# Performance work log

Measured on AMD Instinct MI355X. Metric: run time of the kernel, lower is better.

## Reference

```python
import jax, jax.numpy as jnp
import numpy as np

N_NODES = 100000
N_EDGES = 1600000
IN_CH, HID_CH, OUT_CH = 128, 64, 40


def setup_inputs() -> dict:
    key = jax.random.key(0)
    k_x, k_e, k_w1, k_w2 = jax.random.split(key, 4)
    x = jax.random.normal(k_x, (N_NODES, IN_CH), dtype=jnp.float32)
    edge_index = jax.random.randint(k_e, (2, N_EDGES), 0, N_NODES, dtype=jnp.int64)
    # Glorot-ish scaled weights, zero bias (matches GCNConv init convention)
    W1 = jax.random.normal(k_w1, (IN_CH, HID_CH), dtype=jnp.float32) / np.sqrt(IN_CH)
    b1 = jnp.zeros((HID_CH,), dtype=jnp.float32)
    W2 = jax.random.normal(k_w2, (HID_CH, OUT_CH), dtype=jnp.float32) / np.sqrt(HID_CH)
    b2 = jnp.zeros((OUT_CH,), dtype=jnp.float32)
    return {"x": x, "edge_index": edge_index, "W1": W1, "b1": b1, "W2": W2, "b2": b2}


def _gcn_conv(x, edge_index, W, b, n):
    """GCNConv with normalize=True: linear transform, add self-loops,
    symmetric D^-1/2 A D^-1/2 aggregation (source_to_target flow), bias."""
    h = x @ W  # [n, out]
    loops = jnp.arange(n, dtype=edge_index.dtype)
    row = jnp.concatenate([edge_index[0], loops])  # sources
    col = jnp.concatenate([edge_index[1], loops])  # targets
    deg = jax.ops.segment_sum(jnp.ones_like(col, dtype=h.dtype), col, num_segments=n)
    dinv = jnp.where(deg > 0, jax.lax.rsqrt(deg), jnp.zeros_like(deg))
    w = dinv[row] * dinv[col]  # [E+n] per-edge norm
    out = jax.ops.segment_sum(h[row] * w[:, None], col, num_segments=n)  # scatter-add to targets
    return out + b


def reference(x, edge_index, W1, b1, W2, b2):
    # eval mode: F.dropout(p=0.8, training=False) is identity
    n = x.shape[0]
    h = jax.nn.relu(_gcn_conv(x, edge_index, W1, b1, n))
    return _gcn_conv(h, edge_index, W2, b2, n)  # [N, OUT_CH] logits
```

## Files before the change

kernel.cpp:

```cpp
#include <hip/hip_runtime.h>

#define N_NODES 100000
#define N_EDGES 1600000
#define IN_CH   128
#define HID_CH  64
#define OUT_CH  40
#define NBKT    391
#define EPB     4096
#define CAP     6144

using bf16x8 = __attribute__((ext_vector_type(8))) short;
using f32x4  = __attribute__((ext_vector_type(4))) float;

__device__ __forceinline__ float bf2f(unsigned short u) {
    union { unsigned int i; float f; } c; c.i = ((unsigned int)u) << 16; return c.f;
}
__device__ __forceinline__ unsigned short f2bf(float f) {
    union { float f; unsigned int i; } c; c.f = f;
    unsigned int r = c.i + 0x7FFFu + ((c.i >> 16) & 1u);
    return (unsigned short)(r >> 16);
}
__device__ __forceinline__ float4 bf2f4(ushort4 u) {
    return make_float4(bf2f(u.x), bf2f(u.y), bf2f(u.z), bf2f(u.w));
}

__global__ void k_setup(const float* __restrict__ W1, const float* __restrict__ W2,
                        unsigned short* __restrict__ W1t, unsigned short* __restrict__ W2t,
                        int* __restrict__ gcur) {
    int stride = gridDim.x * blockDim.x;
    int t0 = blockIdx.x * blockDim.x + threadIdx.x;
    if (t0 < NBKT) gcur[t0] = t0 * CAP;
    for (int i = t0; i < 64 * 128; i += stride) {
        int n = i >> 7, k = i & 127;
        W1t[i] = f2bf(W1[k * 64 + n]);
    }
    for (int i = t0; i < 48 * 64; i += stride) {
        int n = i >> 6, k = i & 63;
        W2t[i] = f2bf(n < 40 ? W2[k * 40 + n] : 0.0f);
    }
}

__global__ void k_bin(const int* __restrict__ ei, int* __restrict__ gcur,
                      int* __restrict__ ebuf) {
    __shared__ int hist[NBKT];
    __shared__ int lcur[NBKT];
    int tid = threadIdx.x;
    int base = blockIdx.x * EPB;
    int nloc = N_EDGES - base;
    if (nloc > EPB) nloc = EPB;
    int n4 = nloc >> 2;
    const int4* S4 = (const int4*)(ei + base);
    const int4* D4 = (const int4*)(ei + N_EDGES + base);

    for (int i = tid; i < NBKT; i += 256) hist[i] = 0;
    __syncthreads();
    for (int i = tid; i < n4; i += 256) {
        int4 d = D4[i];
        atomicAdd(&hist[d.x >> 8], 1);
        atomicAdd(&hist[d.y >> 8], 1);
        atomicAdd(&hist[d.z >> 8], 1);
        atomicAdd(&hist[d.w >> 8], 1);
    }
    __syncthreads();
    for (int i = tid; i < NBKT; i += 256) {
        int h = hist[i];
        lcur[i] = h ? atomicAdd(&gcur[i], h) : 0;
    }
    __syncthreads();
    for (int i = tid; i < n4; i += 256) {
        int4 s = S4[i];
        int4 d = D4[i];
        int p;
        p = atomicAdd(&lcur[d.x >> 8], 1); ebuf[p] = s.x | ((d.x & 255) << 20);
        p = atomicAdd(&lcur[d.y >> 8], 1); ebuf[p] = s.y | ((d.y & 255) << 20);
        p = atomicAdd(&lcur[d.z >> 8], 1); ebuf[p] = s.z | ((d.z & 255) << 20);
        p = atomicAdd(&lcur[d.w >> 8], 1); ebuf[p] = s.w | ((d.w & 255) << 20);
    }
}

__global__ void k_node(const int* __restrict__ gcur, const int* __restrict__ ebuf,
                       int* __restrict__ row_start, int* __restrict__ row_end,
                       int* __restrict__ csr_src, float* __restrict__ dinv) {
    __shared__ int cnt[256];
    __shared__ int s[256];
    int tid = threadIdx.x;
    int b = blockIdx.x;
    int node0 = b << 8;
    int lo = b * CAP, hi = gcur[b];
    int n = hi - lo, n4 = n >> 2;
    const int4* E4 = (const int4*)(ebuf + lo);

    cnt[tid] = 0;
    __syncthreads();
    for (int i = tid; i < n4; i += 256) {
        int4 w = E4[i];
        atomicAdd(&cnt[(unsigned)w.x >> 20], 1);
        atomicAdd(&cnt[(unsigned)w.y >> 20], 1);
        atomicAdd(&cnt[(unsigned)w.z >> 20], 1);
        atomicAdd(&cnt[(unsigned)w.w >> 20], 1);
    }
    for (int e = lo + (n4 << 2) + tid; e < hi; e += 256)
        atomicAdd(&cnt[(unsigned)ebuf[e] >> 20], 1);
    __syncthreads();
    int c = cnt[tid];
    s[tid] = c;
    __syncthreads();
#pragma unroll
    for (int off = 1; off < 256; off <<= 1) {
        int tv = (tid >= off) ? s[tid - off] : 0;
        __syncthreads();
        s[tid] += tv;
        __syncthreads();
    }
    int node = node0 + tid;
    if (node < N_NODES) {
        row_start[node] = lo + s[tid] - c;
        row_end[node]   = lo + s[tid];
        dinv[node] = rsqrtf(1.0f + (float)c);
    }
    __syncthreads();
    cnt[tid] = lo + s[tid] - c;
    __syncthreads();
    for (int i = tid; i < n4; i += 256) {
        int4 w = E4[i];
        int p;
        p = atomicAdd(&cnt[(unsigned)w.x >> 20], 1); csr_src[p] = w.x & 0xFFFFF;
        p = atomicAdd(&cnt[(unsigned)w.y >> 20], 1); csr_src[p] = w.y & 0xFFFFF;
        p = atomicAdd(&cnt[(unsigned)w.z >> 20], 1); csr_src[p] = w.z & 0xFFFFF;
        p = atomicAdd(&cnt[(unsigned)w.w >> 20], 1); csr_src[p] = w.w & 0xFFFFF;
    }
    for (int e = lo + (n4 << 2) + tid; e < hi; e += 256) {
        int w = ebuf[e];
        int p = atomicAdd(&cnt[(unsigned)w >> 20], 1);
        csr_src[p] = w & 0xFFFFF;
    }
}

__global__ __launch_bounds__(256, 4)
void k_gemm1(const float* __restrict__ x, const unsigned short* __restrict__ W1t,
             const float* __restrict__ dinv, unsigned short* __restrict__ h1s) {
    __shared__ unsigned short Al[64 * 136];
    __shared__ unsigned short Bl[64 * 136];
    __shared__ float dl[64];
    int tid = threadIdx.x;
    long long node0 = (long long)blockIdx.x * 64;

    const float4* X = (const float4*)x;
    for (int i = tid; i < 64 * 32; i += 256) {
        int r = i >> 5, c4 = i & 31;
        long long gr = node0 + r;
        if (gr >= N_NODES) gr = N_NODES - 1;
        float4 v = X[gr * 32 + c4];
        *(ushort4*)&Al[r * 136 + c4 * 4] =
            make_ushort4(f2bf(v.x), f2bf(v.y), f2bf(v.z), f2bf(v.w));
    }
    for (int i = tid; i < 64 * 16; i += 256) {
        int nn = i >> 4, c8 = i & 15;
        *(ulonglong2*)&Bl[nn * 136 + c8 * 8] = *(const ulonglong2*)&W1t[nn * 128 + c8 * 8];
    }
    if (tid < 64) {
        long long gr = node0 + tid;
        dl[tid] = dinv[gr < N_NODES ? gr : N_NODES - 1];
    }
    __syncthreads();

    int lane = tid & 63, wave = tid >> 6;
    int quad = lane >> 4, l16 = lane & 15;
    int arow = wave * 16 + l16;
    f32x4 ac0 = {0,0,0,0}, ac1 = {0,0,0,0}, ac2 = {0,0,0,0}, ac3 = {0,0,0,0};

#pragma unroll
    for (int ks = 0; ks < 4; ++ks) {
        int ko = ks * 32 + quad * 8;
        bf16x8 a  = *(const bf16x8*)&Al[arow * 136 + ko];
        bf16x8 b0 = *(const bf16x8*)&Bl[( 0 + l16) * 136 + ko];
        bf16x8 b1 = *(const bf16x8*)&Bl[(16 + l16) * 136 + ko];
        bf16x8 b2 = *(const bf16x8*)&Bl[(32 + l16) * 136 + ko];
        bf16x8 b3 = *(const bf16x8*)&Bl[(48 + l16) * 136 + ko];
        ac0 = __builtin_amdgcn_mfma_f32_16x16x32_bf16(a, b0, ac0, 0, 0, 0);
        ac1 = __builtin_amdgcn_mfma_f32_16x16x32_bf16(a, b1, ac1, 0, 0, 0);
        ac2 = __builtin_amdgcn_mfma_f32_16x16x32_bf16(a, b2, ac2, 0, 0, 0);
        ac3 = __builtin_amdgcn_mfma_f32_16x16x32_bf16(a, b3, ac3, 0, 0, 0);
    }

#pragma unroll
    for (int r = 0; r < 4; ++r) {
        int rl = wave * 16 + quad * 4 + r;
        long long grow = node0 + rl;
        if (grow < N_NODES) {
            float dd = dl[rl];
            h1s[grow * 64 +  0 + l16] = f2bf(ac0[r] * dd);
            h1s[grow * 64 + 16 + l16] = f2bf(ac1[r] * dd);
            h1s[grow * 64 + 32 + l16] = f2bf(ac2[r] * dd);
            h1s[grow * 64 + 48 + l16] = f2bf(ac3[r] * dd);
        }
    }
}

__global__ void k_agg1(const int* __restrict__ row_start, const int* __restrict__ row_end,
                       const int* __restrict__ csr_src,
                       const unsigned short* __restrict__ h1s, const float* __restrict__ dinv,
                       const float* __restrict__ b1, unsigned short* __restrict__ a1b) {
    int idx = blockIdx.x * blockDim.x + threadIdx.x;
    int node = idx >> 4;
    int cg = idx & 15;
    if (node >= N_NODES) return;
    int e = row_start[node];
    int f = row_end[node];
    const ushort4* H = (const ushort4*)h1s;
    float4 acc = bf2f4(H[(long long)node * 16 + cg]);
    float4 acc2 = {0.f, 0.f, 0.f, 0.f};
    while (f - e >= 8) {
        int s0 = csr_src[e];
        int s1 = csr_src[e + 1];
        int s2 = csr_src[e + 2];
        int s3 = csr_src[e + 3];
        int t0 = csr_src[f - 4];
        int t1 = csr_src[f - 3];
        int t2 = csr_src[f - 2];
        int t3 = csr_src[f - 1];
        float4 v0 = bf2f4(H[(long long)s0 * 16 + cg]);
        float4 v1 = bf2f4(H[(long long)s1 * 16 + cg]);
        float4 v2 = bf2f4(H[(long long)s2 * 16 + cg]);
        float4 v3 = bf2f4(H[(long long)s3 * 16 + cg]);
        float4 u0 = bf2f4(H[(long long)t0 * 16 + cg]);
        float4 u1 = bf2f4(H[(long long)t1 * 16 + cg]);
        float4 u2 = bf2f4(H[(long long)t2 * 16 + cg]);
        float4 u3 = bf2f4(H[(long long)t3 * 16 + cg]);
        acc.x  += (v0.x + v1.x) + (v2.x + v3.x);
        acc.y  += (v0.y + v1.y) + (v2.y + v3.y);
        acc.z  += (v0.z + v1.z) + (v2.z + v3.z);
        acc.w  += (v0.w + v1.w) + (v2.w + v3.w);
        acc2.x += (u0.x + u1.x) + (u2.x + u3.x);
        acc2.y += (u0.y + u1.y) + (u2.y + u3.y);
        acc2.z += (u0.z + u1.z) + (u2.z + u3.z);
        acc2.w += (u0.w + u1.w) + (u2.w + u3.w);
        e += 4; f -= 4;
    }
    for (; e < f; ++e) {
        float4 v = bf2f4(H[(long long)csr_src[e] * 16 + cg]);
        acc.x += v.x; acc.y += v.y; acc.z += v.z; acc.w += v.w;
    }
    acc.x += acc2.x; acc.y += acc2.y; acc.z += acc2.z; acc.w += acc2.w;
    float dd = dinv[node];
    float4 bb = ((const float4*)b1)[cg];
    float rx = fmaxf(acc.x * dd + bb.x, 0.f);
    float ry = fmaxf(acc.y * dd + bb.y, 0.f);
    float rz = fmaxf(acc.z * dd + bb.z, 0.f);
    float rw = fmaxf(acc.w * dd + bb.w, 0.f);
    ((ushort4*)a1b)[(long long)node * 16 + cg] =
        make_ushort4(f2bf(rx), f2bf(ry), f2bf(rz), f2bf(rw));
}

__global__ __launch_bounds__(256, 4)
void k_gemm2(const unsigned short* __restrict__ a1b, const unsigned short* __restrict__ W2t,
             const float* __restrict__ dinv, unsigned short* __restrict__ h2s) {
    __shared__ unsigned short Al[64 * 72];
    __shared__ unsigned short Bl[48 * 72];
    __shared__ float dl[64];
    int tid = threadIdx.x;
    long long node0 = (long long)blockIdx.x * 64;

    for (int i = tid; i < 64 * 8; i += 256) {
        int r = i >> 3, c8 = i & 7;
        long long gr = node0 + r;
        if (gr >= N_NODES) gr = N_NODES - 1;
        *(ulonglong2*)&Al[r * 72 + c8 * 8] = *(const ulonglong2*)&a1b[gr * 64 + c8 * 8];
    }
    for (int i = tid; i < 48 * 8; i += 256) {
        int nn = i >> 3, c8 = i & 7;
        *(ulonglong2*)&Bl[nn * 72 + c8 * 8] = *(const ulonglong2*)&W2t[nn * 64 + c8 * 8];
    }
    if (tid < 64) {
        long long gr = node0 + tid;
        dl[tid] = dinv[gr < N_NODES ? gr : N_NODES - 1];
    }
    __syncthreads();

    int lane = tid & 63, wave = tid >> 6;
    int quad = lane >> 4, l16 = lane & 15;
    int arow = wave * 16 + l16;
    f32x4 ac0 = {0,0,0,0}, ac1 = {0,0,0,0}, ac2 = {0,0,0,0};

#pragma unroll
    for (int ks = 0; ks < 2; ++ks) {
        int ko = ks * 32 + quad * 8;
        bf16x8 a  = *(const bf16x8*)&Al[arow * 72 + ko];
        bf16x8 b0 = *(const bf16x8*)&Bl[( 0 + l16) * 72 + ko];
        bf16x8 b1v = *(const bf16x8*)&Bl[(16 + l16) * 72 + ko];
        bf16x8 b2 = *(const bf16x8*)&Bl[(32 + l16) * 72 + ko];
        ac0 = __builtin_amdgcn_mfma_f32_16x16x32_bf16(a, b0, ac0, 0, 0, 0);
        ac1 = __builtin_amdgcn_mfma_f32_16x16x32_bf16(a, b1v, ac1, 0, 0, 0);
        ac2 = __builtin_amdgcn_mfma_f32_16x16x32_bf16(a, b2, ac2, 0, 0, 0);
    }

#pragma unroll
    for (int r = 0; r < 4; ++r) {
        int rl = wave * 16 + quad * 4 + r;
        long long grow = node0 + rl;
        if (grow < N_NODES) {
            float dd = dl[rl];
            h2s[grow * 40 +  0 + l16] = f2bf(ac0[r] * dd);
            h2s[grow * 40 + 16 + l16] = f2bf(ac1[r] * dd);
            if (l16 < 8) h2s[grow * 40 + 32 + l16] = f2bf(ac2[r] * dd);
        }
    }
}

__global__ void k_agg2(const int* __restrict__ row_start, const int* __restrict__ row_end,
                       const int* __restrict__ csr_src,
                       const unsigned short* __restrict__ h2s, const float* __restrict__ dinv,
                       const float* __restrict__ b2, float* __restrict__ out) {
    int idx = blockIdx.x * blockDim.x + threadIdx.x;
    int node = idx >> 4;
    int cg = idx & 15;
    if (node >= N_NODES || cg >= 10) return;
    int e = row_start[node];
    int f = row_end[node];
    const ushort4* H = (const ushort4*)h2s;
    float4 acc = bf2f4(H[(long long)node * 10 + cg]);
    float4 acc2 = {0.f, 0.f, 0.f, 0.f};
    while (f - e >= 8) {
        int s0 = csr_src[e];
        int s1 = csr_src[e + 1];
        int s2 = csr_src[e + 2];
        int s3 = csr_src[e + 3];
        int t0 = csr_src[f - 4];
        int t1 = csr_src[f - 3];
        int t2 = csr_src[f - 2];
        int t3 = csr_src[f - 1];
        float4 v0 = bf2f4(H[(long long)s0 * 10 + cg]);
        float4 v1 = bf2f4(H[(long long)s1 * 10 + cg]);
        float4 v2 = bf2f4(H[(long long)s2 * 10 + cg]);
        float4 v3 = bf2f4(H[(long long)s3 * 10 + cg]);
        float4 u0 = bf2f4(H[(long long)t0 * 10 + cg]);
        float4 u1 = bf2f4(H[(long long)t1 * 10 + cg]);
        float4 u2 = bf2f4(H[(long long)t2 * 10 + cg]);
        float4 u3 = bf2f4(H[(long long)t3 * 10 + cg]);
        acc.x  += (v0.x + v1.x) + (v2.x + v3.x);
        acc.y  += (v0.y + v1.y) + (v2.y + v3.y);
        acc.z  += (v0.z + v1.z) + (v2.z + v3.z);
        acc.w  += (v0.w + v1.w) + (v2.w + v3.w);
        acc2.x += (u0.x + u1.x) + (u2.x + u3.x);
        acc2.y += (u0.y + u1.y) + (u2.y + u3.y);
        acc2.z += (u0.z + u1.z) + (u2.z + u3.z);
        acc2.w += (u0.w + u1.w) + (u2.w + u3.w);
        e += 4; f -= 4;
    }
    for (; e < f; ++e) {
        float4 v = bf2f4(H[(long long)csr_src[e] * 10 + cg]);
        acc.x += v.x; acc.y += v.y; acc.z += v.z; acc.w += v.w;
    }
    acc.x += acc2.x; acc.y += acc2.y; acc.z += acc2.z; acc.w += acc2.w;
    float dd = dinv[node];
    float4 b = ((const float4*)b2)[cg];
    acc.x = acc.x * dd + b.x;
    acc.y = acc.y * dd + b.y;
    acc.z = acc.z * dd + b.z;
    acc.w = acc.w * dd + b.w;
    ((float4*)out)[(long long)node * 10 + cg] = acc;
}

extern "C" void kernel_launch(void* const* d_in, const int* in_sizes, int n_in,
                              void* d_out, int out_size, void* d_ws, size_t ws_size,
                              hipStream_t stream) {
    const float* x  = (const float*)d_in[0];
    const int*   ei = (const int*)d_in[1];
    const float* W1 = (const float*)d_in[2];
    const float* b1 = (const float*)d_in[3];
    const float* W2 = (const float*)d_in[4];
    const float* b2 = (const float*)d_in[5];
    float* out = (float*)d_out;

    unsigned short* hbuf = (unsigned short*)d_ws;
    unsigned short* a1b  = hbuf + 64LL * N_NODES;
    int* ebuf      = (int*)(a1b + 64LL * N_NODES);
    int* csr_src   = ebuf + NBKT * CAP;
    int* row_start = csr_src + NBKT * CAP;
    int* row_end   = row_start + N_NODES;
    int* gcur      = row_end + N_NODES;
    float* dinv    = (float*)(gcur + 400);
    unsigned short* W1t = (unsigned short*)(dinv + N_NODES);
    unsigned short* W2t = W1t + 64 * 128;

    const int B = 256;
    const int g16 = (N_NODES * 16 + B - 1) / B;
    const int gRows = (N_NODES + 63) / 64;

    k_setup<<<34, B, 0, stream>>>(W1, W2, W1t, W2t, gcur);
    k_bin<<<(N_EDGES + EPB - 1) / EPB, B, 0, stream>>>(ei, gcur, ebuf);
    k_node<<<NBKT, B, 0, stream>>>(gcur, ebuf, row_start, row_end, csr_src, dinv);

    k_gemm1<<<gRows, B, 0, stream>>>(x, W1t, dinv, hbuf);
    k_agg1<<<g16, B, 0, stream>>>(row_start, row_end, csr_src, hbuf, dinv, b1, a1b);

    k_gemm2<<<gRows, B, 0, stream>>>(a1b, W2t, dinv, hbuf);
    k_agg2<<<g16, B, 0, stream>>>(row_start, row_end, csr_src, hbuf, dinv, b2, out);
}
```

Measured before the change: 226.5 us.

## Fuse layer-1 aggregation with layer-2 GEMM, widen CSR buckets, drop setup kernel

Layer-1 aggregation now writes its ReLU output straight into LDS, and the layer-2 MFMA GEMM consumes it in the same kernel. This removes the a1b round trip through global memory and one kernel launch. Buckets for CSR construction now cover 512 nodes, with k_node running 512 threads per block. The weight-transpose setup kernel is replaced by a memset of per-bucket counters, and each GEMM block converts the fp32 weights itself. The trade-off is extra per-block weight conversion with scattered 2-byte LDS writes, and less parallelism in the fused aggregation, since each thread handles four nodes in sequence.

Result: no change. 225.4 us (-0.5%).

```diff
diff --git a/kernel.cpp b/kernel.cpp
--- a/kernel.cpp
+++ b/kernel.cpp
@@ -5,9 +5,9 @@
 #define IN_CH   128
 #define HID_CH  64
 #define OUT_CH  40
-#define NBKT    391
+#define NBKT    196
 #define EPB     4096
-#define CAP     6144
+#define CAP     9216
 
 using bf16x8 = __attribute__((ext_vector_type(8))) short;
 using f32x4  = __attribute__((ext_vector_type(4))) float;
@@ -22,22 +22,6 @@
 }
 __device__ __forceinline__ float4 bf2f4(ushort4 u) {
     return make_float4(bf2f(u.x), bf2f(u.y), bf2f(u.z), bf2f(u.w));
-}
-
-__global__ void k_setup(const float* __restrict__ W1, const float* __restrict__ W2,
-                        unsigned short* __restrict__ W1t, unsigned short* __restrict__ W2t,
-                        int* __restrict__ gcur) {
-    int stride = gridDim.x * blockDim.x;
-    int t0 = blockIdx.x * blockDim.x + threadIdx.x;
-    if (t0 < NBKT) gcur[t0] = t0 * CAP;
-    for (int i = t0; i < 64 * 128; i += stride) {
-        int n = i >> 7, k = i & 127;
-        W1t[i] = f2bf(W1[k * 64 + n]);
-    }
-    for (int i = t0; i < 48 * 64; i += stride) {
-        int n = i >> 6, k = i & 63;
-        W2t[i] = f2bf(n < 40 ? W2[k * 40 + n] : 0.0f);
-    }
 }
 
 __global__ void k_bin(const int* __restrict__ ei, int* __restrict__ gcur,
@@ -52,61 +36,62 @@
     const int4* S4 = (const int4*)(ei + base);
     const int4* D4 = (const int4*)(ei + N_EDGES + base);
 
-    for (int i = tid; i < NBKT; i += 256) hist[i] = 0;
+    if (tid < NBKT) { hist[tid] = 0; }
     __syncthreads();
     for (int i = tid; i < n4; i += 256) {
         int4 d = D4[i];
-        atomicAdd(&hist[d.x >> 8], 1);
-        atomicAdd(&hist[d.y >> 8], 1);
-        atomicAdd(&hist[d.z >> 8], 1);
-        atomicAdd(&hist[d.w >> 8], 1);
-    }
-    __syncthreads();
-    for (int i = tid; i < NBKT; i += 256) {
-        int h = hist[i];
-        lcur[i] = h ? atomicAdd(&gcur[i], h) : 0;
+        atomicAdd(&hist[d.x >> 9], 1);
+        atomicAdd(&hist[d.y >> 9], 1);
+        atomicAdd(&hist[d.z >> 9], 1);
+        atomicAdd(&hist[d.w >> 9], 1);
+    }
+    __syncthreads();
+    if (tid < NBKT) {
+        int h = hist[tid];
+        lcur[tid] = h ? (tid * CAP + atomicAdd(&gcur[tid], h)) : 0;
     }
     __syncthreads();
     for (int i = tid; i < n4; i += 256) {
         int4 s = S4[i];
         int4 d = D4[i];
         int p;
-        p = atomicAdd(&lcur[d.x >> 8], 1); ebuf[p] = s.x | ((d.x & 255) << 20);
-        p = atomicAdd(&lcur[d.y >> 8], 1); ebuf[p] = s.y | ((d.y & 255) << 20);
-        p = atomicAdd(&lcur[d.z >> 8], 1); ebuf[p] = s.z | ((d.z & 255) << 20);
-        p = atomicAdd(&lcur[d.w >> 8], 1); ebuf[p] = s.w | ((d.w & 255) << 20);
+        p = atomicAdd(&lcur[d.x >> 9], 1); ebuf[p] = s.x | ((d.x & 511) << 17);
+        p = atomicAdd(&lcur[d.y >> 9], 1); ebuf[p] = s.y | ((d.y & 511) << 17);
+        p = atomicAdd(&lcur[d.z >> 9], 1); ebuf[p] = s.z | ((d.z & 511) << 17);
+        p = atomicAdd(&lcur[d.w >> 9], 1); ebuf[p] = s.w | ((d.w & 511) << 17);
     }
 }
 
 __global__ void k_node(const int* __restrict__ gcur, const int* __restrict__ ebuf,
                        int* __restrict__ row_start, int* __restrict__ row_end,
                        int* __restrict__ csr_src, float* __restrict__ dinv) {
-    __shared__ int cnt[256];
-    __shared__ int s[256];
+    __shared__ int cnt[512];
+    __shared__ int s[512];
     int tid = threadIdx.x;
     int b = blockIdx.x;
-    int node0 = b << 8;
-    int lo = b * CAP, hi = gcur[b];
+    int node0 = b << 9;
+    int lo = b * CAP;
+    int hi = lo + gcur[b];
     int n = hi - lo, n4 = n >> 2;
     const int4* E4 = (const int4*)(ebuf + lo);
 
     cnt[tid] = 0;
     __syncthreads();
-    for (int i = tid; i < n4; i += 256) {
+    for (int i = tid; i < n4; i += 512) {
         int4 w = E4[i];
-        atomicAdd(&cnt[(unsigned)w.x >> 20], 1);
-        atomicAdd(&cnt[(unsigned)w.y >> 20], 1);
-        atomicAdd(&cnt[(unsigned)w.z >> 20], 1);
-        atomicAdd(&cnt[(unsigned)w.w >> 20], 1);
-    }
-    for (int e = lo + (n4 << 2) + tid; e < hi; e += 256)
-        atomicAdd(&cnt[(unsigned)ebuf[e] >> 20], 1);
+        atomicAdd(&cnt[(unsigned)w.x >> 17], 1);
+        atomicAdd(&cnt[(unsigned)w.y >> 17], 1);
+        atomicAdd(&cnt[(unsigned)w.z >> 17], 1);
+        atomicAdd(&cnt[(unsigned)w.w >> 17], 1);
+    }
+    for (int e = lo + (n4 << 2) + tid; e < hi; e += 512)
+        atomicAdd(&cnt[(unsigned)ebuf[e] >> 17], 1);
     __syncthreads();
     int c = cnt[tid];
     s[tid] = c;
     __syncthreads();
 #pragma unroll
-    for (int off = 1; off < 256; off <<= 1) {
+    for (int off = 1; off < 512; off <<= 1) {
         int tv = (tid >= off) ? s[tid - off] : 0;
         __syncthreads();
         s[tid] += tv;
@@ -121,23 +106,23 @@
     __syncthreads();
     cnt[tid] = lo + s[tid] - c;
     __syncthreads();
-    for (int i = tid; i < n4; i += 256) {
+    for (int i = tid; i < n4; i += 512) {
         int4 w = E4[i];
         int p;
-        p = atomicAdd(&cnt[(unsigned)w.x >> 20], 1); csr_src[p] = w.x & 0xFFFFF;
-        p = atomicAdd(&cnt[(unsigned)w.y >> 20], 1); csr_src[p] = w.y & 0xFFFFF;
-        p = atomicAdd(&cnt[(unsigned)w.z >> 20], 1); csr_src[p] = w.z & 0xFFFFF;
-        p = atomicAdd(&cnt[(unsigned)w.w >> 20], 1); csr_src[p] = w.w & 0xFFFFF;
-    }
-    for (int e = lo + (n4 << 2) + tid; e < hi; e += 256) {
+        p = atomicAdd(&cnt[(unsigned)w.x >> 17], 1); csr_src[p] = w.x & 0x1FFFF;
+        p = atomicAdd(&cnt[(unsigned)w.y >> 17], 1); csr_src[p] = w.y & 0x1FFFF;
+        p = atomicAdd(&cnt[(unsigned)w.z >> 17], 1); csr_src[p] = w.z & 0x1FFFF;
+        p = atomicAdd(&cnt[(unsigned)w.w >> 17], 1); csr_src[p] = w.w & 0x1FFFF;
+    }
+    for (int e = lo + (n4 << 2) + tid; e < hi; e += 512) {
         int w = ebuf[e];
-        int p = atomicAdd(&cnt[(unsigned)w >> 20], 1);
-        csr_src[p] = w & 0xFFFFF;
+        int p = atomicAdd(&cnt[(unsigned)w >> 17], 1);
+        csr_src[p] = w & 0x1FFFF;
     }
 }
 
 __global__ __launch_bounds__(256, 4)
-void k_gemm1(const float* __restrict__ x, const unsigned short* __restrict__ W1t,
+void k_gemm1(const float* __restrict__ x, const float* __restrict__ W1,
              const float* __restrict__ dinv, unsigned short* __restrict__ h1s) {
     __shared__ unsigned short Al[64 * 136];
     __shared__ unsigned short Bl[64 * 136];
@@ -154,9 +139,9 @@
         *(ushort4*)&Al[r * 136 + c4 * 4] =
             make_ushort4(f2bf(v.x), f2bf(v.y), f2bf(v.z), f2bf(v.w));
     }
-    for (int i = tid; i < 64 * 16; i += 256) {
-        int nn = i >> 4, c8 = i & 15;
-        *(ulonglong2*)&Bl[nn * 136 + c8 * 8] = *(const ulonglong2*)&W1t[nn * 128 + c8 * 8];
+    for (int i = tid; i < 128 * 64; i += 256) {
+        int k = i >> 6, nn = i & 63;
+        Bl[nn * 136 + k] = f2bf(W1[i]);
     }
     if (tid < 64) {
         long long gr = node0 + tid;
@@ -197,83 +182,82 @@
     }
 }
 
-__global__ void k_agg1(const int* __restrict__ row_start, const int* __restrict__ row_end,
-                       const int* __restrict__ csr_src,
-                       const unsigned short* __restrict__ h1s, const float* __restrict__ dinv,
-                       const float* __restrict__ b1, unsigned short* __restrict__ a1b) {
-    int idx = blockIdx.x * blockDim.x + threadIdx.x;
-    int node = idx >> 4;
-    int cg = idx & 15;
-    if (node >= N_NODES) return;
-    int e = row_start[node];
-    int f = row_end[node];
-    const ushort4* H = (const ushort4*)h1s;
-    float4 acc = bf2f4(H[(long long)node * 16 + cg]);
-    float4 acc2 = {0.f, 0.f, 0.f, 0.f};
-    while (f - e >= 8) {
-        int s0 = csr_src[e];
-        int s1 = csr_src[e + 1];
-        int s2 = csr_src[e + 2];
-        int s3 = csr_src[e + 3];
-        int t0 = csr_src[f - 4];
-        int t1 = csr_src[f - 3];
-        int t2 = csr_src[f - 2];
-        int t3 = csr_src[f - 1];
-        float4 v0 = bf2f4(H[(long long)s0 * 16 + cg]);
-        float4 v1 = bf2f4(H[(long long)s1 * 16 + cg]);
-        float4 v2 = bf2f4(H[(long long)s2 * 16 + cg]);
-        float4 v3 = bf2f4(H[(long long)s3 * 16 + cg]);
-        float4 u0 = bf2f4(H[(long long)t0 * 16 + cg]);
-        float4 u1 = bf2f4(H[(long long)t1 * 16 + cg]);
-        float4 u2 = bf2f4(H[(long long)t2 * 16 + cg]);
-        float4 u3 = bf2f4(H[(long long)t3 * 16 + cg]);
-        acc.x  += (v0.x + v1.x) + (v2.x + v3.x);
-        acc.y  += (v0.y + v1.y) + (v2.y + v3.y);
-        acc.z  += (v0.z + v1.z) + (v2.z + v3.z);
-        acc.w  += (v0.w + v1.w) + (v2.w + v3.w);
-        acc2.x += (u0.x + u1.x) + (u2.x + u3.x);
-        acc2.y += (u0.y + u1.y) + (u2.y + u3.y);
-        acc2.z += (u0.z + u1.z) + (u2.z + u3.z);
-        acc2.w += (u0.w + u1.w) + (u2.w + u3.w);
-        e += 4; f -= 4;
-    }
-    for (; e < f; ++e) {
-        float4 v = bf2f4(H[(long long)csr_src[e] * 16 + cg]);
-        acc.x += v.x; acc.y += v.y; acc.z += v.z; acc.w += v.w;
-    }
-    acc.x += acc2.x; acc.y += acc2.y; acc.z += acc2.z; acc.w += acc2.w;
-    float dd = dinv[node];
-    float4 bb = ((const float4*)b1)[cg];
-    float rx = fmaxf(acc.x * dd + bb.x, 0.f);
-    float ry = fmaxf(acc.y * dd + bb.y, 0.f);
-    float rz = fmaxf(acc.z * dd + bb.z, 0.f);
-    float rw = fmaxf(acc.w * dd + bb.w, 0.f);
-    ((ushort4*)a1b)[(long long)node * 16 + cg] =
-        make_ushort4(f2bf(rx), f2bf(ry), f2bf(rz), f2bf(rw));
-}
-
 __global__ __launch_bounds__(256, 4)
-void k_gemm2(const unsigned short* __restrict__ a1b, const unsigned short* __restrict__ W2t,
-             const float* __restrict__ dinv, unsigned short* __restrict__ h2s) {
+void k_agg1g2(const int* __restrict__ row_start, const int* __restrict__ row_end,
+              const int* __restrict__ csr_src,
+              const unsigned short* __restrict__ h1s, const float* __restrict__ dinv,
+              const float* __restrict__ b1, const float* __restrict__ W2,
+              unsigned short* __restrict__ h2s) {
     __shared__ unsigned short Al[64 * 72];
     __shared__ unsigned short Bl[48 * 72];
     __shared__ float dl[64];
     int tid = threadIdx.x;
     long long node0 = (long long)blockIdx.x * 64;
 
-    for (int i = tid; i < 64 * 8; i += 256) {
-        int r = i >> 3, c8 = i & 7;
-        long long gr = node0 + r;
-        if (gr >= N_NODES) gr = N_NODES - 1;
-        *(ulonglong2*)&Al[r * 72 + c8 * 8] = *(const ulonglong2*)&a1b[gr * 64 + c8 * 8];
-    }
-    for (int i = tid; i < 48 * 8; i += 256) {
-        int nn = i >> 3, c8 = i & 7;
-        *(ulonglong2*)&Bl[nn * 72 + c8 * 8] = *(const ulonglong2*)&W2t[nn * 64 + c8 * 8];
+    for (int i = tid; i < 48 * 64; i += 256) {
+        int nn = i >> 6, k = i & 63;
+        Bl[nn * 72 + k] = f2bf(nn < OUT_CH ? W2[k * OUT_CH + nn] : 0.0f);
     }
     if (tid < 64) {
         long long gr = node0 + tid;
         dl[tid] = dinv[gr < N_NODES ? gr : N_NODES - 1];
+    }
+    __syncthreads();
+
+    int cg = tid & 15;
+    int nsub = tid >> 4;
+    float4 bb = ((const float4*)b1)[cg];
+    const ushort4* H = (const ushort4*)h1s;
+
+#pragma unroll
+    for (int r4 = 0; r4 < 4; ++r4) {
+        int nl = r4 * 16 + nsub;
+        long long node = node0 + nl;
+        ushort4 res = make_ushort4(0, 0, 0, 0);
+        if (node < N_NODES) {
+            int e = row_start[node];
+            int f = row_end[node];
+            float4 acc = bf2f4(H[node * 16 + cg]);
+            float4 acc2 = {0.f, 0.f, 0.f, 0.f};
+            while (f - e >= 8) {
+                int s0 = csr_src[e];
+                int s1 = csr_src[e + 1];
+                int s2 = csr_src[e + 2];
+                int s3 = csr_src[e + 3];
+                int t0 = csr_src[f - 4];
+                int t1 = csr_src[f - 3];
+                int t2 = csr_src[f - 2];
+                int t3 = csr_src[f - 1];
+                float4 v0 = bf2f4(H[(long long)s0 * 16 + cg]);
+                float4 v1 = bf2f4(H[(long long)s1 * 16 + cg]);
+                float4 v2 = bf2f4(H[(long long)s2 * 16 + cg]);
+                float4 v3 = bf2f4(H[(long long)s3 * 16 + cg]);
+                float4 u0 = bf2f4(H[(long long)t0 * 16 + cg]);
+                float4 u1 = bf2f4(H[(long long)t1 * 16 + cg]);
+                float4 u2 = bf2f4(H[(long long)t2 * 16 + cg]);
+                float4 u3 = bf2f4(H[(long long)t3 * 16 + cg]);
+                acc.x  += (v0.x + v1.x) + (v2.x + v3.x);
+                acc.y  += (v0.y + v1.y) + (v2.y + v3.y);
+                acc.z  += (v0.z + v1.z) + (v2.z + v3.z);
+                acc.w  += (v0.w + v1.w) + (v2.w + v3.w);
+                acc2.x += (u0.x + u1.x) + (u2.x + u3.x);
+                acc2.y += (u0.y + u1.y) + (u2.y + u3.y);
+                acc2.z += (u0.z + u1.z) + (u2.z + u3.z);
+                acc2.w += (u0.w + u1.w) + (u2.w + u3.w);
+                e += 4; f -= 4;
+            }
+            for (; e < f; ++e) {
+                float4 v = bf2f4(H[(long long)csr_src[e] * 16 + cg]);
+                acc.x += v.x; acc.y += v.y; acc.z += v.z; acc.w += v.w;
+            }
+            acc.x += acc2.x; acc.y += acc2.y; acc.z += acc2.z; acc.w += acc2.w;
+            float dd = dl[nl];
+            res = make_ushort4(f2bf(fmaxf(acc.x * dd + bb.x, 0.f)),
+                               f2bf(fmaxf(acc.y * dd + bb.y, 0.f)),
+                               f2bf(fmaxf(acc.z * dd + bb.z, 0.f)),
+                               f2bf(fmaxf(acc.w * dd + bb.w, 0.f)));
+        }
+        *(ushort4*)&Al[nl * 72 + cg * 4] = res;
     }
     __syncthreads();
 
@@ -372,28 +356,25 @@
     const float* b2 = (const float*)d_in[5];
     float* out = (float*)d_out;
 
-    unsigned short* hbuf = (unsigned short*)d_ws;
-    unsigned short* a1b  = hbuf + 64LL * N_NODES;
-    int* ebuf      = (int*)(a1b + 64LL * N_NODES);
+    unsigned short* hbuf  = (unsigned short*)d_ws;
+    unsigned short* h2buf = hbuf + 64LL * N_NODES;
+    int* ebuf      = (int*)(h2buf + 64LL * N_NODES);
     int* csr_src   = ebuf + NBKT * CAP;
     int* row_start = csr_src + NBKT * CAP;
     int* row_end   = row_start + N_NODES;
     int* gcur      = row_end + N_NODES;
-    float* dinv    = (float*)(gcur + 400);
-    unsigned short* W1t = (unsigned short*)(dinv + N_NODES);
-    unsigned short* W2t = W1t + 64 * 128;
+    float* dinv    = (float*)(gcur + 256);
 
     const int B = 256;
     const int g16 = (N_NODES * 16 + B - 1) / B;
     const int gRows = (N_NODES + 63) / 64;
 
-    k_setup<<<34, B, 0, stream>>>(W1, W2, W1t, W2t, gcur);
+    hipMemsetAsync((void*)gcur, 0, NBKT * sizeof(int), stream);
     k_bin<<<(N_EDGES + EPB - 1) / EPB, B, 0, stream>>>(ei, gcur, ebuf);
-    k_node<<<NBKT, B, 0, stream>>>(gcur, ebuf, row_start, row_end, csr_src, dinv);
-
-    k_gemm1<<<gRows, B, 0, stream>>>(x, W1t, dinv, hbuf);
-    k_agg1<<<g16, B, 0, stream>>>(row_start, row_end, csr_src, hbuf, dinv, b1, a1b);
-
-    k_gemm2<<<gRows, B, 0, stream>>>(a1b, W2t, dinv, hbuf);
-    k_agg2<<<g16, B, 0, stream>>>(row_start, row_end, csr_src, hbuf, dinv, b2, out);
-}
+    k_node<<<NBKT, 512, 0, stream>>>(gcur, ebuf, row_start, row_end, csr_src, dinv);
+
+    k_gemm1<<<gRows, B, 0, stream>>>(x, W1, dinv, hbuf);
+    k_agg1g2<<<gRows, B, 0, stream>>>(row_start, row_end, csr_src, hbuf, dinv,
+                                      b1, W2, h2buf);
+    k_agg2<<<g16, B, 0, stream>>>(row_start, row_end, csr_src, h2buf, dinv, b2, out);
+}
```
